# Performance work log

Hardware: AMD Instinct MI355X
Metric: run time of the kernel (lower is better)

## Reference

```python
import jax, jax.numpy as jnp
import numpy as np
from jax import lax

D_VOCAB = 262
D_EMB = 128
CONV_W = 5
PAD = CONV_W // 2  # 2


def setup_inputs() -> dict:
    key = jax.random.key(0)
    k1, k2, k3, k4, k5 = jax.random.split(key, 5)
    B, W, C = 128, 256, 16
    input = jax.random.randint(k1, (B, W, C), 0, D_VOCAB, dtype=jnp.int64)
    lengths = jax.random.randint(k2, (B, W), 1, C + 1, dtype=jnp.int64)
    # torch init: Embedding weight ~ N(0,1) then *0.1
    emb_weight = jax.random.normal(k3, (D_VOCAB, D_EMB), dtype=jnp.float32) * 0.1
    fan_in = D_EMB * CONV_W
    bound = 1.0 / np.sqrt(fan_in)
    conv_w = jax.random.uniform(k4, (D_EMB, D_EMB, CONV_W), dtype=jnp.float32, minval=-bound, maxval=bound)
    conv_b = jax.random.uniform(k5, (D_EMB,), dtype=jnp.float32, minval=-bound, maxval=bound)
    return {"input": input, "lengths": lengths, "emb_weight": emb_weight,
            "conv_w": conv_w, "conv_b": conv_b}


def reference(input, lengths, emb_weight, conv_w, conv_b):
    B, W, C = input.shape
    ids = input.reshape(B * W, C)                      # [N, C]
    embed = emb_weight[ids]                            # [N, C, E] gather
    x = jnp.transpose(embed, (0, 2, 1))                # [N, E, C] (NCW)
    y = lax.conv_general_dilated(
        x, conv_w,
        window_strides=(1,), padding=[(PAD, PAD)],
        dimension_numbers=("NCH", "OIH", "NCH"))       # [N, E, C]
    y = y + conv_b[None, :, None]
    out = jnp.max(y, axis=-1)                          # max-pool over chars
    return out.reshape(B, W, -1)                       # [B, W, E]
```

## Files before the change

kernel.cpp:

```cpp
#include <hip/hip_runtime.h>
#include <hip/hip_fp16.h>

#define D_VOCAB 262
#define D_EMB   128
#define KW      5
#define NCHAR   16
#define NKO     (KW * D_EMB)

typedef _Float16 h2 __attribute__((ext_vector_type(2)));
typedef _Float16 h8 __attribute__((ext_vector_type(8)));


__global__ __launch_bounds__(256) void transpose_w_kernel(
    const float* __restrict__ cw, float* __restrict__ Wt2) {
  const int gid = blockIdx.x * 256 + threadIdx.x;
  const float val = cw[gid];
  const int o = gid / 640;
  const int r = gid - o * 640;
  const int i = r / 5;
  const int k = r - i * 5;
  Wt2[i * NKO + k * D_EMB + o] = val;
}

__global__ __launch_bounds__(640) void compute_P_kernel(
    const float* __restrict__ emb, const float* __restrict__ Wt2,
    __half* __restrict__ P) {
  __shared__ float emb_s[D_EMB];
  const int v = blockIdx.x;
  const int t = threadIdx.x;
  if (t < D_EMB) emb_s[t] = emb[v * D_EMB + t];
  __syncthreads();

  const float* col = Wt2 + t;
  float a0 = 0.f, a1 = 0.f;
#pragma unroll 8
  for (int i = 0; i < D_EMB; i += 2) {
    a0 += emb_s[i]     * col[i * NKO];
    a1 += emb_s[i + 1] * col[(i + 1) * NKO];
  }
  P[v * NKO + t] = __float2half(a0 + a1);
}

#define CH       16
#define NQ       (D_EMB / CH)
#define VSTRIDE  176
#define LDS_SZ   (D_VOCAB * VSTRIDE)
#define SEQ_PER_BLOCK 512

__global__ __launch_bounds__(1024) void conv_char_main_kernel(
    const int* __restrict__ ids, const _Float16* __restrict__ P,
    const float* __restrict__ bias, float* __restrict__ out) {
  __shared__ __attribute__((aligned(16))) char Plds[LDS_SZ];

  const int tid  = threadIdx.x;
  const int lane = tid & 63;
  const int wid  = tid >> 6;
  const int q    = blockIdx.x >> 6;
  const int sb   = blockIdx.x & 63;

  for (int u = tid; u < LDS_SZ / 16; u += 1024) {
    const int L = u * 16;
    const int v = L / VSTRIDE;
    const int r = L - v * VSTRIDE;
    if (r < 160) {
      const h8 val = *(const h8*)(P + v * NKO + (r >> 5) * D_EMB + q * CH + ((r & 31) >> 1));
      *(h8*)(Plds + L) = val;
    }
  }
  __syncthreads();

  const int grp = lane >> 1;
  const int t   = lane & 1;
  const int seq = sb * SEQ_PER_BLOCK + wid * 32 + grp;

  const int4* idp = (const int4*)(ids + seq * NCHAR);
  const int4 ia = idp[0];
  const int4 ib = idp[1];
  const int4 ic = idp[2];
  const int4 id4 = idp[3];

  h8 win[5];
#pragma unroll
  for (int w = 0; w < 5; ++w) win[w] = (h8)(_Float16)0.f;
  h8 vmax = (h8)(_Float16)(-60000.f);

  const char* Pl = Plds + t * 16;

#pragma unroll
  for (int j = 0; j < NCHAR; ++j) {
    const int idj = (j < 4)  ? ((const int*)&ia)[j & 3]
                  : (j < 8)  ? ((const int*)&ib)[j & 3]
                  : (j < 12) ? ((const int*)&ic)[j & 3]
                             : ((const int*)&id4)[j & 3];
    const char* row = Pl + idj * VSTRIDE;
#pragma unroll
    for (int k = 0; k < KW; ++k) {
      const int c = j + 2 - k;
      if (c >= 0 && c < NCHAR) {
        const h8 val = *(const h8*)(row + k * 32);
        win[c % 5] += val;
      }
    }
    if (j >= 2) {
      const int w = (j - 2) % 5;
      vmax = __builtin_elementwise_max(vmax, win[w]);
      win[w] = (h8)(_Float16)0.f;
    }
  }
  vmax = __builtin_elementwise_max(vmax, win[14 % 5]);
  vmax = __builtin_elementwise_max(vmax, win[15 % 5]);

  const int o = q * CH + t * 8;
  const float4 b0 = *(const float4*)(bias + o);
  const float4 b1 = *(const float4*)(bias + o + 4);
  float* op = out + (size_t)seq * D_EMB + o;
  float4 r0, r1;
  r0.x = (float)vmax[0] + b0.x;
  r0.y = (float)vmax[1] + b0.y;
  r0.z = (float)vmax[2] + b0.z;
  r0.w = (float)vmax[3] + b0.w;
  r1.x = (float)vmax[4] + b1.x;
  r1.y = (float)vmax[5] + b1.y;
  r1.z = (float)vmax[6] + b1.z;
  r1.w = (float)vmax[7] + b1.w;
  *(float4*)op = r0;
  *(float4*)(op + 4) = r1;
}

extern "C" void kernel_launch(void* const* d_in, const int* in_sizes, int n_in,
                              void* d_out, int out_size, void* d_ws, size_t ws_size,
                              hipStream_t stream) {
  const int*   input = (const int*)d_in[0];
  const float* emb   = (const float*)d_in[2];
  const float* cw    = (const float*)d_in[3];
  const float* cb    = (const float*)d_in[4];
  float* out = (float*)d_out;

  _Float16* P   = (_Float16*)d_ws;
  float*    Wt2 = (float*)((char*)d_ws + 335872);

  const int n_seq = in_sizes[0] / NCHAR;

  transpose_w_kernel<<<320, 256, 0, stream>>>(cw, Wt2);
  compute_P_kernel<<<D_VOCAB, 640, 0, stream>>>(emb, Wt2, (__half*)P);

  const int nsb = n_seq / SEQ_PER_BLOCK;
  conv_char_main_kernel<<<NQ * nsb, 1024, 0, stream>>>(input, P, cb, out);
}
```

Baseline: 92.38 us.

## Fuse weight transpose and P precompute into one LDS-tiled kernel

```diff
diff --git a/kernel.cpp b/kernel.cpp
--- a/kernel.cpp
+++ b/kernel.cpp
@@ -11,34 +11,59 @@
 typedef _Float16 h8 __attribute__((ext_vector_type(8)));
 
 
-__global__ __launch_bounds__(256) void transpose_w_kernel(
-    const float* __restrict__ cw, float* __restrict__ Wt2) {
-  const int gid = blockIdx.x * 256 + threadIdx.x;
-  const float val = cw[gid];
-  const int o = gid / 640;
-  const int r = gid - o * 640;
-  const int i = r / 5;
-  const int k = r - i * 5;
-  Wt2[i * NKO + k * D_EMB + o] = val;
-}
+#define VG 8
+#define OT 32
+#define BT_PAD 33
 
-__global__ __launch_bounds__(640) void compute_P_kernel(
-    const float* __restrict__ emb, const float* __restrict__ Wt2,
+__global__ __launch_bounds__(256) void fused_P_kernel(
+    const float* __restrict__ emb, const float* __restrict__ cw,
     __half* __restrict__ P) {
-  __shared__ float emb_s[D_EMB];
-  const int v = blockIdx.x;
-  const int t = threadIdx.x;
-  if (t < D_EMB) emb_s[t] = emb[v * D_EMB + t];
+  __shared__ float Btile[NKO * BT_PAD];
+  __shared__ float emb_s[VG][D_EMB];
+
+  const int tid = threadIdx.x;
+  const int ot  = blockIdx.x & 3;
+  const int vg  = blockIdx.x >> 2;
+  const int o0  = ot * OT;
+  const int v0  = vg * VG;
+
+  const float* slab = cw + o0 * NKO;
+  for (int u = tid; u < OT * NKO; u += 256) {
+    const int oc = u / NKO;
+    const int r  = u - oc * NKO;
+    Btile[r * BT_PAD + oc] = slab[u];
+  }
+  for (int u = tid; u < VG * D_EMB; u += 256) {
+    const int vr  = u >> 7;
+    const int col = u & 127;
+    const int v   = v0 + vr;
+    emb_s[vr][col] = (v < D_VOCAB) ? emb[v * D_EMB + col] : 0.f;
+  }
   __syncthreads();
 
-  const float* col = Wt2 + t;
-  float a0 = 0.f, a1 = 0.f;
-#pragma unroll 8
-  for (int i = 0; i < D_EMB; i += 2) {
-    a0 += emb_s[i]     * col[i * NKO];
-    a1 += emb_s[i + 1] * col[(i + 1) * NKO];
+  if (tid < KW * OT) {
+    const int k  = tid >> 5;
+    const int oc = tid & 31;
+    const float* colp = Btile + k * BT_PAD + oc;
+
+    float acc[VG];
+#pragma unroll
+    for (int vr = 0; vr < VG; ++vr) acc[vr] = 0.f;
+
+#pragma unroll 4
+    for (int i = 0; i < D_EMB; ++i) {
+      const float b = colp[i * (KW * BT_PAD)];
+#pragma unroll
+      for (int vr = 0; vr < VG; ++vr) acc[vr] += emb_s[vr][i] * b;
+    }
+
+#pragma unroll
+    for (int vr = 0; vr < VG; ++vr) {
+      const int v = v0 + vr;
+      if (v < D_VOCAB)
+        P[v * NKO + k * D_EMB + o0 + oc] = __float2half(acc[vr]);
+    }
   }
-  P[v * NKO + t] = __float2half(a0 + a1);
 }
 
 #define CH       16
@@ -136,13 +161,11 @@
   const float* cb    = (const float*)d_in[4];
   float* out = (float*)d_out;
 
-  _Float16* P   = (_Float16*)d_ws;
-  float*    Wt2 = (float*)((char*)d_ws + 335872);
+  _Float16* P = (_Float16*)d_ws;
 
   const int n_seq = in_sizes[0] / NCHAR;
 
-  transpose_w_kernel<<<320, 256, 0, stream>>>(cw, Wt2);
-  compute_P_kernel<<<D_VOCAB, 640, 0, stream>>>(emb, Wt2, (__half*)P);
+  fused_P_kernel<<<4 * 33, 256, 0, stream>>>(emb, cw, (__half*)P);
 
   const int nsb = n_seq / SEQ_PER_BLOCK;
   conv_char_main_kernel<<<NQ * nsb, 1024, 0, stream>>>(input, P, cb, out);
```

After: 95.38 us. 1.03x slower.
